# Performance work log

Measured on AMD Instinct MI355X. Metric: run time of the kernel, lower is better.

Reference implementation:

```python
import jax, jax.numpy as jnp
import numpy as np

INFEATURES = 4096
OUTFEATURES = 11008
GROUP_SIZE = 128
N_GROUPS = INFEATURES // GROUP_SIZE  # 32
PACK = 8  # 32 bits / 4 bits


def _unpack_int4(packed):
    # packed: [R, C//8] int32 -> [R, C] int32 nibbles in [0, 15]
    shifts = (jnp.arange(PACK, dtype=jnp.int32) * 4)
    nib = (packed[:, :, None] >> shifts[None, None, :]) & 0xF
    return nib.reshape(packed.shape[0], packed.shape[1] * PACK)


def setup_inputs() -> dict:
    key = jax.random.key(0)
    k1, k2, k3, k4, k5 = jax.random.split(key, 5)
    x = jax.random.normal(k1, (2048, INFEATURES), dtype=jnp.float32)
    qweight = jax.random.randint(k2, (INFEATURES, OUTFEATURES // PACK), 0, 2147483647, dtype=jnp.int32)
    qzeros = jax.random.randint(k3, (N_GROUPS, OUTFEATURES // PACK), 0, 2147483647, dtype=jnp.int32)
    scales = jax.random.uniform(k4, (N_GROUPS, OUTFEATURES), minval=0.001, maxval=0.01, dtype=jnp.float32)
    bias = jax.random.normal(k5, (OUTFEATURES,), dtype=jnp.float32) * 0.01
    return {"x": x, "qweight": qweight, "qzeros": qzeros, "scales": scales, "bias": bias}


def reference(x, qweight, qzeros, scales, bias):
    # convert_from_uint4: dequantize packed int4 weight with per-group scale/zero
    w_int = _unpack_int4(qweight)                       # [in, out] int4 values
    z_int = _unpack_int4(qzeros)                        # [n_groups, out]
    dt = scales.dtype
    # broadcast group params to per-row (trivial g_idx: row i -> group i // GROUP_SIZE)
    z = jnp.repeat(z_int.astype(dt), GROUP_SIZE, axis=0)      # [in, out]
    s = jnp.repeat(scales, GROUP_SIZE, axis=0)                # [in, out]
    weight = (w_int.astype(dt) - z) * s                       # [in, out]
    out = jnp.matmul(x, weight) + bias                        # [tokens, out]
    return out
```

## Files before the change

### kernel.cpp

```cpp
#include <hip/hip_runtime.h>

typedef __bf16 bf16_t;
typedef bf16_t bf16x8 __attribute__((ext_vector_type(8)));
typedef float  floatx4 __attribute__((ext_vector_type(4)));
typedef unsigned int uint;

constexpr int Mdim = 2048;
constexpr int Kdim = 4096;
constexpr int Ndim = 11008;
constexpr int NPK  = Ndim / 8;
constexpr int SQ   = 68;
constexpr int BM = 128, BN = 128, BK = 64;
constexpr int SA = 72, SB = 72;

#define GLOAD_LDS16(g, l) \
    __builtin_amdgcn_global_load_lds((const __attribute__((address_space(1))) void*)(g), \
                                     (__attribute__((address_space(3))) void*)(l), 16, 0, 0)
#define MFMA(a, b, c) __builtin_amdgcn_mfma_f32_16x16x32_bf16((a), (b), (c), 0, 0, 0)
#define BAR()    __builtin_amdgcn_s_barrier()
#define LGKM0()  asm volatile("s_waitcnt lgkmcnt(0)" ::: "memory")
#define VMCNT2() asm volatile("s_waitcnt vmcnt(2)" ::: "memory")
#define PRIO1()  __builtin_amdgcn_s_setprio(1)
#define PRIO0()  __builtin_amdgcn_s_setprio(0)

__global__ void xcast_kernel(const float* __restrict__ x, bf16_t* __restrict__ xb)
{
    const int i = (blockIdx.x * 256 + threadIdx.x) * 8;
    const float4 a = *(const float4*)(x + i);
    const float4 b = *(const float4*)(x + i + 4);
    bf16x8 v;
    v[0] = (bf16_t)a.x; v[1] = (bf16_t)a.y; v[2] = (bf16_t)a.z; v[3] = (bf16_t)a.w;
    v[4] = (bf16_t)b.x; v[5] = (bf16_t)b.y; v[6] = (bf16_t)b.z; v[7] = (bf16_t)b.w;
    *(bf16x8*)(xb + i) = v;
}

__global__ __launch_bounds__(256, 4)
void wdeq_kernel(const uint* __restrict__ qweight, const uint* __restrict__ qzeros,
                 const float* __restrict__ scales, bf16_t* __restrict__ wt)
{
    __shared__ uint qbuf[16 * SQ];
    const int t  = threadIdx.x;
    const int n0 = blockIdx.x * 128;
    const int k0 = blockIdx.y * 64;
    const int c0 = n0 >> 3;
    const int g  = k0 >> 7;

    const int qk  = t >> 2;
    const int qc4 = (t & 3) * 4;
    const uint4 w4 = *(const uint4*)(qweight + (size_t)(k0 + qk) * NPK + c0 + qc4);
    qbuf[(qc4 + 0) * SQ + qk] = w4.x;
    qbuf[(qc4 + 1) * SQ + qk] = w4.y;
    qbuf[(qc4 + 2) * SQ + qk] = w4.z;
    qbuf[(qc4 + 3) * SQ + qk] = w4.w;
    __syncthreads();

    const int kcol = t & 7;
    const int nr   = t >> 3;
    const int jsh  = (nr & 7) * 4;
#pragma unroll
    for (int j = 0; j < 4; ++j) {
        const int row = nr + j * 32;
        const int cc  = row >> 3;
        const uint  zw = qzeros[(size_t)g * NPK + c0 + cc];
        const float s  = scales[(size_t)g * Ndim + n0 + row];
        const float zs = (float)((zw >> jsh) & 15u) * s;
        const uint* qrow = &qbuf[cc * SQ + kcol * 8];
        const uint4 qa = *(const uint4*)(qrow);
        const uint4 qb = *(const uint4*)(qrow + 4);
        bf16x8 v;
        v[0] = (bf16_t)((float)((qa.x >> jsh) & 15u) * s - zs);
        v[1] = (bf16_t)((float)((qa.y >> jsh) & 15u) * s - zs);
        v[2] = (bf16_t)((float)((qa.z >> jsh) & 15u) * s - zs);
        v[3] = (bf16_t)((float)((qa.w >> jsh) & 15u) * s - zs);
        v[4] = (bf16_t)((float)((qb.x >> jsh) & 15u) * s - zs);
        v[5] = (bf16_t)((float)((qb.y >> jsh) & 15u) * s - zs);
        v[6] = (bf16_t)((float)((qb.z >> jsh) & 15u) * s - zs);
        v[7] = (bf16_t)((float)((qb.w >> jsh) & 15u) * s - zs);
        *(bf16x8*)(wt + (size_t)(n0 + row) * Kdim + k0 + kcol * 8) = v;
    }
}

__global__ __launch_bounds__(512, 2)
void gemm8_kernel(const bf16_t* __restrict__ xb, const bf16_t* __restrict__ wt,
                  const float* __restrict__ bias, float* __restrict__ out)
{
    __shared__ bf16_t As[2 * 16384];
    __shared__ bf16_t Bs[2 * 8192];

    const int t    = threadIdx.x;
    const int w    = t >> 6;
    const int lane = t & 63;
    const int quad = lane >> 4;
    const int l16  = lane & 15;
    const int wm   = w >> 2;
    const int wn   = (w >> 1) & 1;
    const int wk   = w & 1;
    const int w64  = w * 64;

    const int flat = blockIdx.y * 86 + blockIdx.x;
    const int nf   = (flat & 7) * 86 + (flat >> 3);
    const int m0   = (nf / 86) * 256;
    const int n0   = (nf % 86) * 128;

    auto stageA = [&](int T, int h) {
        const int p  = T & 1;
        const int Tk = (T & 63) * 64;
#pragma unroll
        for (int l = 0; l < 2; ++l) {
            const int idx = l * 512 + w64 + lane;
            const int r   = idx >> 3;
            const int bc  = (idx & 7) ^ (r & 7);
            GLOAD_LDS16(xb + (size_t)(m0 + h * 128 + r) * Kdim + Tk + bc * 8,
                        As + (p * 16384 + h * 8192 + (l * 512 + w64) * 8));
        }
    };
    auto stageB = [&](int T) {
        const int p  = T & 1;
        const int Tk = (T & 63) * 64;
#pragma unroll
        for (int l = 0; l < 2; ++l) {
            const int idx = l * 512 + w64 + lane;
            const int r   = idx >> 3;
            const int bc  = (idx & 7) ^ (r & 7);
            GLOAD_LDS16(wt + (size_t)(n0 + r) * Kdim + Tk + bc * 8,
                        Bs + (p * 8192 + (l * 512 + w64) * 8));
        }
    };
    auto lda = [&](int p, int mt) -> bf16x8 {
        const int r = mt * 16 + l16;
        return *(const bf16x8*)(As + p * 16384 + wm * 8192 + r * 64 +
                                ((wk * 4 + quad) ^ (l16 & 7)) * 8);
    };
    auto ldb = [&](int p, int nt) -> bf16x8 {
        const int r = wn * 64 + nt * 16 + l16;
        return *(const bf16x8*)(Bs + p * 8192 + r * 64 +
                                ((wk * 4 + quad) ^ (l16 & 7)) * 8);
    };

    floatx4 acc[8][4];
#pragma unroll
    for (int i = 0; i < 8; ++i)
#pragma unroll
        for (int j = 0; j < 4; ++j)
            acc[i][j] = (floatx4){0.f, 0.f, 0.f, 0.f};

    stageA(0, 0); stageA(0, 1); stageB(0); stageB(1);
    VMCNT2(); BAR();

    bf16x8 av[4], bb[4];

#define MFMA16(G)                                                              \
    PRIO1();                                                                   \
    _Pragma("unroll") for (int mt = 0; mt < 4; ++mt)                           \
        _Pragma("unroll") for (int nt = 0; nt < 4; ++nt)                       \
            acc[(G)*4 + mt][nt] = MFMA(av[mt], bb[nt], acc[(G)*4 + mt][nt]);   \
    PRIO0();

    for (int i = 0; i < 32; ++i) {
        bb[0] = ldb(0, 0); bb[1] = ldb(0, 1); bb[2] = ldb(0, 2); bb[3] = ldb(0, 3);
        av[0] = lda(0, 0); av[1] = lda(0, 1); av[2] = lda(0, 2); av[3] = lda(0, 3);
        stageA(2 * i + 1, 0); stageA(2 * i + 1, 1);
        BAR(); LGKM0();
        MFMA16(0);
        BAR();

        av[0] = lda(0, 4); av[1] = lda(0, 5); av[2] = lda(0, 6); av[3] = lda(0, 7);
        stageB(2 * i + 2);
        VMCNT2();
        BAR(); LGKM0();
        MFMA16(1);
        BAR();

        bb[0] = ldb(1, 0); bb[1] = ldb(1, 1); bb[2] = ldb(1, 2); bb[3] = ldb(1, 3);
        av[0] = lda(1, 0); av[1] = lda(1, 1); av[2] = lda(1, 2); av[3] = lda(1, 3);
        stageA(2 * i + 2, 0); stageA(2 * i + 2, 1);
        BAR(); LGKM0();
        MFMA16(0);
        BAR();

        av[0] = lda(1, 4); av[1] = lda(1, 5); av[2] = lda(1, 6); av[3] = lda(1, 7);
        stageB(2 * i + 3);
        VMCNT2();
        BAR(); LGKM0();
        MFMA16(1);
        BAR();
    }
#undef MFMA16

    {
        float* exf = (float*)As;
        const int pw = w ^ 1;
#pragma unroll
        for (int c = 0; c < 2; ++c) {
            if (wk == 0) {
#pragma unroll
                for (int q = 0; q < 2; ++q)
#pragma unroll
                    for (int nt = 0; nt < 4; ++nt)
                        *(floatx4*)(exf + w * 2048 + ((q * 4 + nt) * 64 + lane) * 4) =
                            acc[4 + c * 2 + q][nt];
            } else {
#pragma unroll
                for (int q = 0; q < 2; ++q)
#pragma unroll
                    for (int nt = 0; nt < 4; ++nt)
                        *(floatx4*)(exf + w * 2048 + ((q * 4 + nt) * 64 + lane) * 4) =
                            acc[c * 2 + q][nt];
            }
            __syncthreads();
            if (wk == 0) {
#pragma unroll
                for (int q = 0; q < 2; ++q)
#pragma unroll
                    for (int nt = 0; nt < 4; ++nt)
                        acc[c * 2 + q][nt] += *(const floatx4*)(exf + pw * 2048 +
                                                ((q * 4 + nt) * 64 + lane) * 4);
            } else {
#pragma unroll
                for (int q = 0; q < 2; ++q)
#pragma unroll
                    for (int nt = 0; nt < 4; ++nt)
                        acc[4 + c * 2 + q][nt] += *(const floatx4*)(exf + pw * 2048 +
                                                ((q * 4 + nt) * 64 + lane) * 4);
            }
            __syncthreads();
        }
    }

    if (wk == 0) {
#pragma unroll
        for (int nt = 0; nt < 4; ++nt) {
            const int col = n0 + wn * 64 + nt * 16 + l16;
            const float bv = bias[col];
#pragma unroll
            for (int q = 0; q < 4; ++q)
#pragma unroll
                for (int r = 0; r < 4; ++r) {
                    const int row = m0 + wm * 128 + q * 16 + quad * 4 + r;
                    out[(size_t)row * Ndim + col] = acc[q][nt][r] + bv;
                }
        }
    } else {
#pragma unroll
        for (int nt = 0; nt < 4; ++nt) {
            const int col = n0 + wn * 64 + nt * 16 + l16;
            const float bv = bias[col];
#pragma unroll
            for (int q = 0; q < 4; ++q)
#pragma unroll
                for (int r = 0; r < 4; ++r) {
                    const int row = m0 + wm * 128 + (4 + q) * 16 + quad * 4 + r;
                    out[(size_t)row * Ndim + col] = acc[4 + q][nt][r] + bv;
                }
        }
    }
}

template <bool PRE>
__global__ __launch_bounds__(256, 3)
void qgemm_kernel(const float* __restrict__ x,
                  const bf16_t* __restrict__ xb,
                  const uint* __restrict__ qweight,
                  const uint* __restrict__ qzeros,
                  const float* __restrict__ scales,
                  const float* __restrict__ bias,
                  float* __restrict__ out)
{
    __shared__ bf16_t As[BM * SA];
    __shared__ bf16_t Bs[BN * SB];
    __shared__ uint   qbuf[16 * SQ];

    const int t  = threadIdx.x;
    const int m0 = blockIdx.y * BM;
    const int n0 = blockIdx.x * BN;
    const int c0 = n0 >> 3;

    const int wave = t >> 6;
    const int lane = t & 63;
    const int quad = lane >> 4;
    const int l16  = lane & 15;
    const int mw = (wave >> 1) * 64;
    const int nw = (wave & 1) * 64;

    floatx4 acc[4][4];
#pragma unroll
    for (int i = 0; i < 4; ++i)
#pragma unroll
        for (int j = 0; j < 4; ++j)
            acc[i][j] = (floatx4){0.f, 0.f, 0.f, 0.f};

    const int am = t >> 3;
    const int ao = t & 7;
    const int qk  = t >> 2;
    const int qc4 = (t & 3) * 4;
    const int nloc  = t & 127;
    const int khalf = t >> 7;
    const int cc    = nloc >> 3;
    const int jsh   = (nloc & 7) * 4;

    for (int kt = 0; kt < Kdim / BK; ++kt) {
        const int k0 = kt * BK;
        const int g  = k0 >> 7;

#pragma unroll
        for (int p = 0; p < 4; ++p) {
            const int m = p * 32 + am;
            if (PRE) {
                const bf16x8 v = *(const bf16x8*)(xb + (size_t)(m0 + m) * Kdim + k0 + ao * 8);
                *(bf16x8*)&As[m * SA + ao * 8] = v;
            } else {
                const float* src = x + (size_t)(m0 + m) * Kdim + k0 + ao * 8;
                const float4 a = *(const float4*)src;
                const float4 b = *(const float4*)(src + 4);
                bf16x8 v;
                v[0] = (bf16_t)a.x; v[1] = (bf16_t)a.y; v[2] = (bf16_t)a.z; v[3] = (bf16_t)a.w;
                v[4] = (bf16_t)b.x; v[5] = (bf16_t)b.y; v[6] = (bf16_t)b.z; v[7] = (bf16_t)b.w;
                *(bf16x8*)&As[m * SA + ao * 8] = v;
            }
        }
        {
            const uint4 w4 = *(const uint4*)(qweight + (size_t)(k0 + qk) * NPK + c0 + qc4);
            qbuf[(qc4 + 0) * SQ + qk] = w4.x;
            qbuf[(qc4 + 1) * SQ + qk] = w4.y;
            qbuf[(qc4 + 2) * SQ + qk] = w4.z;
            qbuf[(qc4 + 3) * SQ + qk] = w4.w;
        }
        __syncthreads();

        {
            const uint  zw = qzeros[(size_t)g * NPK + c0 + cc];
            const float s  = scales[(size_t)g * Ndim + n0 + nloc];
            const float zs = (float)((zw >> jsh) & 15u) * s;
            const uint* qrow = &qbuf[cc * SQ + khalf * 32];
#pragma unroll
            for (int j = 0; j < 4; ++j) {
                const uint4 qa = *(const uint4*)(qrow + j * 8);
                const uint4 qb = *(const uint4*)(qrow + j * 8 + 4);
                bf16x8 v;
                v[0] = (bf16_t)((float)((qa.x >> jsh) & 15u) * s - zs);
                v[1] = (bf16_t)((float)((qa.y >> jsh) & 15u) * s - zs);
                v[2] = (bf16_t)((float)((qa.z >> jsh) & 15u) * s - zs);
                v[3] = (bf16_t)((float)((qa.w >> jsh) & 15u) * s - zs);
                v[4] = (bf16_t)((float)((qb.x >> jsh) & 15u) * s - zs);
                v[5] = (bf16_t)((float)((qb.y >> jsh) & 15u) * s - zs);
                v[6] = (bf16_t)((float)((qb.z >> jsh) & 15u) * s - zs);
                v[7] = (bf16_t)((float)((qb.w >> jsh) & 15u) * s - zs);
                *(bf16x8*)&Bs[nloc * SB + khalf * 32 + j * 8] = v;
            }
        }
        __syncthreads();

#pragma unroll
        for (int s = 0; s < 2; ++s) {
            bf16x8 fa[4], fb[4];
#pragma unroll
            for (int mt = 0; mt < 4; ++mt)
                fa[mt] = *(const bf16x8*)&As[(mw + mt * 16 + l16) * SA + s * 32 + quad * 8];
#pragma unroll
            for (int nt = 0; nt < 4; ++nt)
                fb[nt] = *(const bf16x8*)&Bs[(nw + nt * 16 + l16) * SB + s * 32 + quad * 8];
#pragma unroll
            for (int mt = 0; mt < 4; ++mt)
#pragma unroll
                for (int nt = 0; nt < 4; ++nt)
                    acc[mt][nt] = MFMA(fa[mt], fb[nt], acc[mt][nt]);
        }
        __syncthreads();
    }

#pragma unroll
    for (int nt = 0; nt < 4; ++nt) {
        const int col = n0 + nw + nt * 16 + l16;
        const float b = bias[col];
#pragma unroll
        for (int mt = 0; mt < 4; ++mt) {
#pragma unroll
            for (int r = 0; r < 4; ++r) {
                const int row = m0 + mw + mt * 16 + quad * 4 + r;
                out[(size_t)row * Ndim + col] = acc[mt][nt][r] + b;
            }
        }
    }
}

extern "C" void kernel_launch(void* const* d_in, const int* in_sizes, int n_in,
                              void* d_out, int out_size, void* d_ws, size_t ws_size,
                              hipStream_t stream)
{
    const float* x        = (const float*)d_in[0];
    const uint*  qweight  = (const uint*)d_in[1];
    const uint*  qzeros   = (const uint*)d_in[2];
    const float* scales   = (const float*)d_in[3];
    const float* bias     = (const float*)d_in[4];
    float*       out      = (float*)d_out;

    const size_t wb_bytes = (size_t)Kdim * Ndim * sizeof(bf16_t);
    const size_t xb_bytes = (size_t)Mdim * Kdim * sizeof(bf16_t);

    if (ws_size >= wb_bytes + xb_bytes) {
        bf16_t* wt = (bf16_t*)d_ws;
        bf16_t* xbuf = (bf16_t*)((char*)d_ws + wb_bytes);
        wdeq_kernel<<<dim3(Ndim / 128, Kdim / 64), 256, 0, stream>>>(qweight, qzeros, scales, wt);
        xcast_kernel<<<(Mdim * Kdim) / (256 * 8), 256, 0, stream>>>(x, xbuf);
        gemm8_kernel<<<dim3(86, 8), dim3(512), 0, stream>>>(xbuf, wt, bias, out);
    } else {
        bf16_t* xbuf = (bf16_t*)d_ws;
        dim3 ggrid(Ndim / BN, Mdim / BM);
        if (ws_size >= xb_bytes) {
            xcast_kernel<<<(Mdim * Kdim) / (256 * 8), 256, 0, stream>>>(x, xbuf);
            qgemm_kernel<true><<<ggrid, dim3(256), 0, stream>>>(x, xbuf, qweight, qzeros, scales, bias, out);
        } else {
            qgemm_kernel<false><<<ggrid, dim3(256), 0, stream>>>(x, xbuf, qweight, qzeros, scales, bias, out);
        }
    }
}
```

Measured before the change: 363.4 us.

## Fuse x cast into weight dequant kernel and triple-buffer GEMM K-loop

Merges the x-to-bf16 cast into the weight dequantization kernel, saving one launch and letting both memory-bound passes share a grid. The GEMM main loop moves from a double-buffered schedule with four barriers per tile to a three-stage LDS ring with prefetch distance two and a single barrier per K tile. The aim is to hide global-to-LDS latency and cut synchronization. The cost is 50% more LDS per block, which may affect occupancy, and fewer explicit lgkm waits, leaving ordering to the compiler.

```diff
diff --git a/kernel.cpp b/kernel.cpp
--- a/kernel.cpp
+++ b/kernel.cpp
@@ -18,8 +18,7 @@
                                      (__attribute__((address_space(3))) void*)(l), 16, 0, 0)
 #define MFMA(a, b, c) __builtin_amdgcn_mfma_f32_16x16x32_bf16((a), (b), (c), 0, 0, 0)
 #define BAR()    __builtin_amdgcn_s_barrier()
-#define LGKM0()  asm volatile("s_waitcnt lgkmcnt(0)" ::: "memory")
-#define VMCNT2() asm volatile("s_waitcnt vmcnt(2)" ::: "memory")
+#define VMCNT6() asm volatile("s_waitcnt vmcnt(6)" ::: "memory")
 #define PRIO1()  __builtin_amdgcn_s_setprio(1)
 #define PRIO0()  __builtin_amdgcn_s_setprio(0)
 
@@ -35,15 +34,25 @@
 }
 
 __global__ __launch_bounds__(256, 4)
-void wdeq_kernel(const uint* __restrict__ qweight, const uint* __restrict__ qzeros,
-                 const float* __restrict__ scales, bf16_t* __restrict__ wt)
+void wprep_kernel(const uint* __restrict__ qweight, const uint* __restrict__ qzeros,
+                  const float* __restrict__ scales, bf16_t* __restrict__ wt,
+                  const float* __restrict__ x, bf16_t* __restrict__ xb)
 {
     __shared__ uint qbuf[16 * SQ];
-    const int t  = threadIdx.x;
-    const int n0 = blockIdx.x * 128;
-    const int k0 = blockIdx.y * 64;
-    const int c0 = n0 >> 3;
-    const int g  = k0 >> 7;
+    const int t    = threadIdx.x;
+    const int n0   = blockIdx.x * 128;
+    const int k0   = blockIdx.y * 64;
+    const int c0   = n0 >> 3;
+    const int g    = k0 >> 7;
+    const int flat = blockIdx.y * 86 + blockIdx.x;
+
+    const int xi = flat * 256 + t;
+    const bool xdo = xi < (Mdim * Kdim) / 8;
+    float4 xa, xb4;
+    if (xdo) {
+        xa  = *(const float4*)(x + xi * 8);
+        xb4 = *(const float4*)(x + xi * 8 + 4);
+    }
 
     const int qk  = t >> 2;
     const int qc4 = (t & 3) * 4;
@@ -78,14 +87,21 @@
         v[7] = (bf16_t)((float)((qb.w >> jsh) & 15u) * s - zs);
         *(bf16x8*)(wt + (size_t)(n0 + row) * Kdim + k0 + kcol * 8) = v;
     }
+
+    if (xdo) {
+        bf16x8 v;
+        v[0] = (bf16_t)xa.x; v[1] = (bf16_t)xa.y; v[2] = (bf16_t)xa.z; v[3] = (bf16_t)xa.w;
+        v[4] = (bf16_t)xb4.x; v[5] = (bf16_t)xb4.y; v[6] = (bf16_t)xb4.z; v[7] = (bf16_t)xb4.w;
+        *(bf16x8*)(xb + xi * 8) = v;
+    }
 }
 
 __global__ __launch_bounds__(512, 2)
 void gemm8_kernel(const bf16_t* __restrict__ xb, const bf16_t* __restrict__ wt,
                   const float* __restrict__ bias, float* __restrict__ out)
 {
-    __shared__ bf16_t As[2 * 16384];
-    __shared__ bf16_t Bs[2 * 8192];
+    __shared__ bf16_t As[3 * 16384];
+    __shared__ bf16_t Bs[3 * 8192];
 
     const int t    = threadIdx.x;
     const int w    = t >> 6;
@@ -102,8 +118,7 @@
     const int m0   = (nf / 86) * 256;
     const int n0   = (nf % 86) * 128;
 
-    auto stageA = [&](int T, int h) {
-        const int p  = T & 1;
+    auto stageA = [&](int b, int T, int h) {
         const int Tk = (T & 63) * 64;
 #pragma unroll
         for (int l = 0; l < 2; ++l) {
@@ -111,11 +126,10 @@
             const int r   = idx >> 3;
             const int bc  = (idx & 7) ^ (r & 7);
             GLOAD_LDS16(xb + (size_t)(m0 + h * 128 + r) * Kdim + Tk + bc * 8,
-                        As + (p * 16384 + h * 8192 + (l * 512 + w64) * 8));
+                        As + (b * 16384 + h * 8192 + (l * 512 + w64) * 8));
         }
     };
-    auto stageB = [&](int T) {
-        const int p  = T & 1;
+    auto stageB = [&](int b, int T) {
         const int Tk = (T & 63) * 64;
 #pragma unroll
         for (int l = 0; l < 2; ++l) {
@@ -123,17 +137,17 @@
             const int r   = idx >> 3;
             const int bc  = (idx & 7) ^ (r & 7);
             GLOAD_LDS16(wt + (size_t)(n0 + r) * Kdim + Tk + bc * 8,
-                        Bs + (p * 8192 + (l * 512 + w64) * 8));
+                        Bs + (b * 8192 + (l * 512 + w64) * 8));
         }
     };
-    auto lda = [&](int p, int mt) -> bf16x8 {
+    auto lda = [&](int b, int mt) -> bf16x8 {
         const int r = mt * 16 + l16;
-        return *(const bf16x8*)(As + p * 16384 + wm * 8192 + r * 64 +
+        return *(const bf16x8*)(As + b * 16384 + wm * 8192 + r * 64 +
                                 ((wk * 4 + quad) ^ (l16 & 7)) * 8);
     };
-    auto ldb = [&](int p, int nt) -> bf16x8 {
+    auto ldb = [&](int b, int nt) -> bf16x8 {
         const int r = wn * 64 + nt * 16 + l16;
-        return *(const bf16x8*)(Bs + p * 8192 + r * 64 +
+        return *(const bf16x8*)(Bs + b * 8192 + r * 64 +
                                 ((wk * 4 + quad) ^ (l16 & 7)) * 8);
     };
 
@@ -144,8 +158,9 @@
         for (int j = 0; j < 4; ++j)
             acc[i][j] = (floatx4){0.f, 0.f, 0.f, 0.f};
 
-    stageA(0, 0); stageA(0, 1); stageB(0); stageB(1);
-    VMCNT2(); BAR();
+    stageA(0, 0, 0); stageA(0, 0, 1); stageB(0, 0);
+    stageA(1, 1, 0); stageA(1, 1, 1); stageB(1, 1);
+    VMCNT6(); BAR();
 
     bf16x8 av[4], bb[4];
 
@@ -156,34 +171,22 @@
             acc[(G)*4 + mt][nt] = MFMA(av[mt], bb[nt], acc[(G)*4 + mt][nt]);   \
     PRIO0();
 
-    for (int i = 0; i < 32; ++i) {
-        bb[0] = ldb(0, 0); bb[1] = ldb(0, 1); bb[2] = ldb(0, 2); bb[3] = ldb(0, 3);
-        av[0] = lda(0, 0); av[1] = lda(0, 1); av[2] = lda(0, 2); av[3] = lda(0, 3);
-        stageA(2 * i + 1, 0); stageA(2 * i + 1, 1);
-        BAR(); LGKM0();
+    int rb = 0;
+    for (int kt = 0; kt < 64; ++kt) {
+        int sb = rb + 2; if (sb >= 3) sb -= 3;
+
+        stageA(sb, kt + 2, 0); stageA(sb, kt + 2, 1);
+        bb[0] = ldb(rb, 0); bb[1] = ldb(rb, 1); bb[2] = ldb(rb, 2); bb[3] = ldb(rb, 3);
+        av[0] = lda(rb, 0); av[1] = lda(rb, 1); av[2] = lda(rb, 2); av[3] = lda(rb, 3);
         MFMA16(0);
+
+        stageB(sb, kt + 2);
+        av[0] = lda(rb, 4); av[1] = lda(rb, 5); av[2] = lda(rb, 6); av[3] = lda(rb, 7);
+        MFMA16(1);
+
+        VMCNT6();
         BAR();
-
-        av[0] = lda(0, 4); av[1] = lda(0, 5); av[2] = lda(0, 6); av[3] = lda(0, 7);
-        stageB(2 * i + 2);
-        VMCNT2();
-        BAR(); LGKM0();
-        MFMA16(1);
-        BAR();
-
-        bb[0] = ldb(1, 0); bb[1] = ldb(1, 1); bb[2] = ldb(1, 2); bb[3] = ldb(1, 3);
-        av[0] = lda(1, 0); av[1] = lda(1, 1); av[2] = lda(1, 2); av[3] = lda(1, 3);
-        stageA(2 * i + 2, 0); stageA(2 * i + 2, 1);
-        BAR(); LGKM0();
-        MFMA16(0);
-        BAR();
-
-        av[0] = lda(1, 4); av[1] = lda(1, 5); av[2] = lda(1, 6); av[3] = lda(1, 7);
-        stageB(2 * i + 3);
-        VMCNT2();
-        BAR(); LGKM0();
-        MFMA16(1);
-        BAR();
+        rb += 1; if (rb >= 3) rb -= 3;
     }
 #undef MFMA16
 
@@ -398,10 +401,9 @@
     const size_t xb_bytes = (size_t)Mdim * Kdim * sizeof(bf16_t);
 
     if (ws_size >= wb_bytes + xb_bytes) {
-        bf16_t* wt = (bf16_t*)d_ws;
+        bf16_t* wt   = (bf16_t*)d_ws;
         bf16_t* xbuf = (bf16_t*)((char*)d_ws + wb_bytes);
-        wdeq_kernel<<<dim3(Ndim / 128, Kdim / 64), 256, 0, stream>>>(qweight, qzeros, scales, wt);
-        xcast_kernel<<<(Mdim * Kdim) / (256 * 8), 256, 0, stream>>>(x, xbuf);
+        wprep_kernel<<<dim3(Ndim / 128, Kdim / 64), 256, 0, stream>>>(qweight, qzeros, scales, wt, x, xbuf);
         gemm8_kernel<<<dim3(86, 8), dim3(512), 0, stream>>>(xbuf, wt, bias, out);
     } else {
         bf16_t* xbuf = (bf16_t*)d_ws;
```

New measurement: 457.8 us. +26.0%, slower.
